# Performance work log

Measured on AMD Instinct MI355X. Metric: run time of the kernel, lower is better.

## Reference

```python
import jax, jax.numpy as jnp
import numpy as np

N_ATOMS = 100000
N_MOLS = 2500
MAX_NB = 10
HID = 256
ATOM_FDIM = 151
FEAT_DIM = 200
FFN_HID = 1024
N_TASKS = 12
LN_EPS = 1e-5


def setup_inputs() -> dict:
    key = jax.random.key(0)
    ks = jax.random.split(key, 12)
    atoms_per_mol = N_ATOMS // N_MOLS  # 40
    starts = jnp.arange(N_MOLS, dtype=jnp.int32) * atoms_per_mol
    sizes = jnp.full((N_MOLS,), atoms_per_mol, dtype=jnp.int32)
    a_scope = jnp.stack([starts, sizes], axis=1)  # [M, 2]
    d_in = HID + ATOM_FDIM  # 407
    d_ff = 4 * HID          # 1024
    d_mol_in = HID + FEAT_DIM  # 456
    def lin(k, fan_in, shape):
        return jax.random.uniform(k, shape, jnp.float32, -1.0, 1.0) / np.sqrt(fan_in)
    return {
        "atom_output": jax.random.normal(ks[0], (N_ATOMS, HID), jnp.float32),
        "original_f_atoms": jax.random.uniform(ks[1], (N_ATOMS, ATOM_FDIM), jnp.float32),
        "a2a": jax.random.randint(ks[2], (N_ATOMS, MAX_NB), 0, N_ATOMS, jnp.int32),
        "a_scope": a_scope,
        "features_batch": jax.random.normal(ks[3], (N_MOLS, FEAT_DIM), jnp.float32),
        "W1": lin(ks[4], d_in, (d_in, d_ff)), "b1": jnp.zeros((d_ff,), jnp.float32),
        "W2": lin(ks[5], d_ff, (d_ff, HID)), "b2": jnp.zeros((HID,), jnp.float32),
        "ln_g": jnp.ones((HID,), jnp.float32), "ln_b": jnp.zeros((HID,), jnp.float32),
        "Wm1": lin(ks[6], d_mol_in, (d_mol_in, FFN_HID)), "bm1": jnp.zeros((FFN_HID,), jnp.float32),
        "Wm2": lin(ks[7], FFN_HID, (FFN_HID, N_TASKS)), "bm2": jnp.zeros((N_TASKS,), jnp.float32),
    }


def reference(atom_output, original_f_atoms, a2a, a_scope, features_batch,
              W1, b1, W2, b2, ln_g, ln_b, Wm1, bm1, Wm2, bm2):
    # select_neighbor_and_aggregate: gather neighbor embeddings and sum
    aggr = atom_output[a2a].sum(axis=1)                      # [N, HID]
    x = jnp.concatenate([original_f_atoms, aggr], axis=1)    # [N, HID+ATOM_FDIM]
    # PositionwiseFeedForward (dropout = identity at eval)
    h = jax.nn.relu(x @ W1 + b1) @ W2 + b2                   # [N, HID]
    # SublayerConnection with x=None: LayerNorm (dropout identity)
    mu = h.mean(axis=-1, keepdims=True)
    var = ((h - mu) ** 2).mean(axis=-1, keepdims=True)
    h = (h - mu) * jax.lax.rsqrt(var + LN_EPS) * ln_g + ln_b
    # Readout: mean over variable-length a_scope ranges (segment mean)
    starts = a_scope[:, 0]
    sizes = a_scope[:, 1]
    n_mols = a_scope.shape[0]
    seg_ids = jnp.searchsorted(starts, jnp.arange(h.shape[0], dtype=starts.dtype), side="right") - 1
    sums = jax.ops.segment_sum(h, seg_ids, num_segments=n_mols)   # [M, HID]
    mol = sums / sizes[:, None].astype(h.dtype)
    # concat molecule-level features, then mol FFN (2 layers)
    mol = jnp.concatenate([mol, features_batch], axis=1)          # [M, HID+FEAT_DIM]
    out = jax.nn.relu(mol @ Wm1 + bm1) @ Wm2 + bm2                # [M, N_TASKS]
    return out
```

## Files before the change

kernel.cpp:

```cpp
#include <hip/hip_runtime.h>

typedef __attribute__((ext_vector_type(8))) short bfrag;
typedef __attribute__((ext_vector_type(4))) float f32x4;

__device__ __forceinline__ float bf2f(unsigned short u) {
    union { unsigned u32; float f; } cv; cv.u32 = ((unsigned)u) << 16; return cv.f;
}
__device__ __forceinline__ unsigned short f2bf(float f) {
    union { float f; unsigned u; } cv; cv.f = f;
    unsigned u = cv.u;
    unsigned r = (u + 0x7fffu + ((u >> 16) & 1u)) >> 16;
    return (unsigned short)r;
}
__device__ __forceinline__ void gll16(const void* g, void* l) {
    __builtin_amdgcn_global_load_lds(
        (const __attribute__((address_space(1))) unsigned int*)g,
        (__attribute__((address_space(3))) unsigned int*)l, 16, 0, 0);
}

__global__ void to_bf16(const float* __restrict__ src, unsigned short* __restrict__ dst, size_t n) {
    size_t i = ((size_t)blockIdx.x * 256 + threadIdx.x) * 8;
    if (i >= n) return;
    float4 a = *reinterpret_cast<const float4*>(src + i);
    float4 b = *reinterpret_cast<const float4*>(src + i + 4);
    ushort4 o0 = {f2bf(a.x), f2bf(a.y), f2bf(a.z), f2bf(a.w)};
    ushort4 o1 = {f2bf(b.x), f2bf(b.y), f2bf(b.z), f2bf(b.w)};
    *reinterpret_cast<ushort4*>(dst + i) = o0;
    *reinterpret_cast<ushort4*>(dst + i + 4) = o1;
}

__global__ void transpose_pad(const float* __restrict__ W, unsigned short* __restrict__ WT,
                              int R, int Cn, int Kp, int split, int shiftA, int split2, int shiftB) {
    __shared__ unsigned short tile[32][33];
    int r0 = blockIdx.x * 32, c0 = blockIdx.y * 32;
#pragma unroll
    for (int j = 0; j < 4; j++) {
        int r = r0 + threadIdx.y + j * 8;
        int c = c0 + threadIdx.x;
        float v = (r < R) ? W[(size_t)r * Cn + c] : 0.f;
        tile[threadIdx.y + j * 8][threadIdx.x] = f2bf(v);
    }
    __syncthreads();
#pragma unroll
    for (int j = 0; j < 4; j++) {
        int c = c0 + threadIdx.y + j * 8;
        int r = r0 + threadIdx.x;
        int kn = (r < split) ? r + shiftA : (r < split2 ? r + shiftB : r);
        WT[(size_t)c * Kp + kn] = tile[threadIdx.x][threadIdx.y + j * 8];
    }
}

__global__ __launch_bounds__(256) void gather2(const unsigned short* __restrict__ abf,
                                               const float* __restrict__ f_atoms,
                                               const int* __restrict__ a2a,
                                               unsigned short* __restrict__ xb, int n_real) {
    int r = blockIdx.x * 4 + (threadIdx.x >> 6);
    int lane = threadIdx.x & 63;
    unsigned short* xrow = xb + (size_t)r * 448;
    if (r >= n_real) {
        *reinterpret_cast<ushort4*>(xrow + lane * 4) = ushort4{0, 0, 0, 0};
        if (lane < 48) *reinterpret_cast<ushort4*>(xrow + 256 + lane * 4) = ushort4{0, 0, 0, 0};
        return;
    }
    int v = (lane < 10) ? a2a[(size_t)r * 10 + lane] : 0;
    ushort4 u[10];
#pragma unroll
    for (int j = 0; j < 10; j++) {
        int nbj = __shfl(v, j);
        u[j] = *reinterpret_cast<const ushort4*>(abf + (size_t)nbj * 256 + lane * 4);
    }
    float a0 = 0.f, a1 = 0.f, a2 = 0.f, a3 = 0.f;
#pragma unroll
    for (int j = 0; j < 10; j++) {
        a0 += bf2f(u[j].x);
        a1 += bf2f(u[j].y);
        a2 += bf2f(u[j].z);
        a3 += bf2f(u[j].w);
    }
    ushort4 o = {f2bf(a0), f2bf(a1), f2bf(a2), f2bf(a3)};
    *reinterpret_cast<ushort4*>(xrow + lane * 4) = o;
    const float* fr = f_atoms + (size_t)r * 151;
#pragma unroll
    for (int s = 0; s < 3; s++) {
        int c = lane + s * 64;
        if (c < 151) xrow[256 + c] = f2bf(fr[c]);
    }
    if (lane < 41) xrow[407 + lane] = 0;
}

template <int RELU>
__global__ __launch_bounds__(256) void gemm97(const unsigned short* __restrict__ A,
                                              const unsigned short* __restrict__ BT,
                                              const float* __restrict__ bias,
                                              unsigned short* __restrict__ C,
                                              int NB, int N, int K) {
    __shared__ __align__(16) unsigned short As[128 * 64];
    __shared__ __align__(16) unsigned short Bs[128 * 64];
    const int t = threadIdx.x;
    const int lane = t & 63, w = t >> 6;
    const int wr = w >> 1, wc = w & 1;
    const int la = lane & 15, hi = lane >> 4;

    const int nwg = gridDim.x, orig = blockIdx.x;
    const int q = nwg >> 3, r8 = nwg & 7;
    const int xcd = orig & 7, slot = orig >> 3;
    const int wgid = (xcd < r8 ? xcd * (q + 1) : r8 * (q + 1) + (xcd - r8) * q) + slot;
    const int bm = (wgid / NB) * 128, bn = (wgid % NB) * 128;

    f32x4 acc[4][4] = {};

    const int trow = t >> 3, tslot = t & 7;
    const unsigned short* Ag = A + (size_t)(bm + trow) * K + (tslot ^ (trow & 7)) * 8;
    const unsigned short* Bg = BT + (size_t)(bn + trow) * K + (tslot ^ (trow & 7)) * 8;
    const int ldst = trow * 64 + tslot * 8;

    for (int kt = 0; kt < K; kt += 64) {
        __builtin_amdgcn_s_barrier();
#pragma unroll
        for (int p = 0; p < 4; p++) gll16(Ag + (size_t)(p * 32) * K + kt, &As[p * 2048 + ldst]);
#pragma unroll
        for (int p = 0; p < 4; p++) gll16(Bg + (size_t)(p * 32) * K + kt, &Bs[p * 2048 + ldst]);
        asm volatile("s_waitcnt vmcnt(0)" ::: "memory");
        __builtin_amdgcn_s_barrier();
#pragma unroll
        for (int kk = 0; kk < 2; kk++) {
            bfrag a[4], b[4];
#pragma unroll
            for (int i = 0; i < 4; i++) {
                int row = wr * 64 + i * 16 + la;
                a[i] = *reinterpret_cast<const bfrag*>(&As[row * 64 + (((kk * 4 + hi) ^ (la & 7)) * 8)]);
            }
#pragma unroll
            for (int j = 0; j < 4; j++) {
                int row = wc * 64 + j * 16 + la;
                b[j] = *reinterpret_cast<const bfrag*>(&Bs[row * 64 + (((kk * 4 + hi) ^ (la & 7)) * 8)]);
            }
#pragma unroll
            for (int i = 0; i < 4; i++)
#pragma unroll
                for (int j = 0; j < 4; j++)
                    acc[i][j] = __builtin_amdgcn_mfma_f32_16x16x32_bf16(a[i], b[j], acc[i][j], 0, 0, 0);
        }
    }

#pragma unroll
    for (int j = 0; j < 4; j++) {
        int col = bn + wc * 64 + j * 16 + la;
        float bv = bias[col];
#pragma unroll
        for (int i = 0; i < 4; i++) {
            int rbase = bm + wr * 64 + i * 16 + hi * 4;
#pragma unroll
            for (int r = 0; r < 4; r++) {
                float v = acc[i][j][r] + bv;
                if (RELU) v = fmaxf(v, 0.f);
                C[(size_t)(rbase + r) * N + col] = f2bf(v);
            }
        }
    }
}

__global__ __launch_bounds__(512) void seg_ln_mean(const unsigned short* __restrict__ h,
                                                   const int* __restrict__ a_scope,
                                                   const float* __restrict__ g,
                                                   const float* __restrict__ b,
                                                   const float* __restrict__ feats,
                                                   unsigned short* __restrict__ mol, int n_mols) {
    __shared__ float part[8][256];
    int m = blockIdx.x, t = threadIdx.x;
    unsigned short* mrow = mol + (size_t)m * 512;
    if (m >= n_mols) {
        mrow[t] = 0;
        return;
    }
    int w = t >> 6, lane = t & 63;
    int start = a_scope[2 * m], size = a_scope[2 * m + 1];
    float4 gv = *reinterpret_cast<const float4*>(g + lane * 4);
    float4 bv = *reinterpret_cast<const float4*>(b + lane * 4);
    float a0 = 0.f, a1 = 0.f, a2 = 0.f, a3 = 0.f;
    for (int r = w; r < size; r += 8) {
        const unsigned short* hp = h + (size_t)(start + r) * 256 + lane * 4;
        ushort4 u = *reinterpret_cast<const ushort4*>(hp);
        float v0 = bf2f(u.x), v1 = bf2f(u.y), v2 = bf2f(u.z), v3 = bf2f(u.w);
        float s = v0 + v1 + v2 + v3;
        float q2 = v0 * v0 + v1 * v1 + v2 * v2 + v3 * v3;
#pragma unroll
        for (int off = 32; off; off >>= 1) {
            s += __shfl_xor(s, off);
            q2 += __shfl_xor(q2, off);
        }
        float mean = s * (1.f / 256.f);
        float var = q2 * (1.f / 256.f) - mean * mean;
        float rs = rsqrtf(var + 1e-5f);
        a0 += (v0 - mean) * rs * gv.x + bv.x;
        a1 += (v1 - mean) * rs * gv.y + bv.y;
        a2 += (v2 - mean) * rs * gv.z + bv.z;
        a3 += (v3 - mean) * rs * gv.w + bv.w;
    }
    part[w][lane * 4 + 0] = a0;
    part[w][lane * 4 + 1] = a1;
    part[w][lane * 4 + 2] = a2;
    part[w][lane * 4 + 3] = a3;
    __syncthreads();
    if (t < 256) {
        float sum = 0.f;
#pragma unroll
        for (int i = 0; i < 8; i++) sum += part[i][t];
        mrow[t] = f2bf(sum / (float)size);
    } else {
        int c = t - 256;
        float fv = (c < 200) ? feats[(size_t)m * 200 + c] : 0.f;
        mrow[256 + c] = f2bf(fv);
    }
}

__global__ void ffn2(const unsigned short* __restrict__ m1, const float* __restrict__ Wm2,
                     const float* __restrict__ bm2, float* __restrict__ out, int n_mols) {
    int wid = blockIdx.x * 4 + (threadIdx.x >> 6);
    if (wid >= n_mols) return;
    int lane = threadIdx.x & 63;
    float acc[12] = {};
    const unsigned short* row = m1 + (size_t)wid * 1024;
#pragma unroll 4
    for (int i = 0; i < 16; i++) {
        int k = i * 64 + lane;
        float v = bf2f(row[k]);
        const float* wr_ = Wm2 + (size_t)k * 12;
#pragma unroll
        for (int tsk = 0; tsk < 12; tsk++) acc[tsk] += v * wr_[tsk];
    }
#pragma unroll
    for (int tsk = 0; tsk < 12; tsk++) {
        float sv = acc[tsk];
#pragma unroll
        for (int off = 32; off; off >>= 1) sv += __shfl_xor(sv, off);
        if (lane == 0) out[(size_t)wid * 12 + tsk] = sv + bm2[tsk];
    }
}

extern "C" void kernel_launch(void* const* d_in, const int* in_sizes, int n_in,
                              void* d_out, int out_size, void* d_ws, size_t ws_size,
                              hipStream_t stream) {
    const float* atom_output = (const float*)d_in[0];
    const float* f_atoms     = (const float*)d_in[1];
    const int*   a2a         = (const int*)d_in[2];
    const int*   a_scope     = (const int*)d_in[3];
    const float* feats       = (const float*)d_in[4];
    const float* W1  = (const float*)d_in[5];
    const float* b1  = (const float*)d_in[6];
    const float* W2  = (const float*)d_in[7];
    const float* b2  = (const float*)d_in[8];
    const float* ln_g = (const float*)d_in[9];
    const float* ln_b = (const float*)d_in[10];
    const float* Wm1 = (const float*)d_in[11];
    const float* bm1 = (const float*)d_in[12];
    const float* Wm2 = (const float*)d_in[13];
    const float* bm2 = (const float*)d_in[14];
    float* out = (float*)d_out;

    char* ws = (char*)d_ws;
    size_t off = 0;
    auto alloc = [&](size_t bytes) {
        void* p = ws + off;
        off += (bytes + 255) & ~(size_t)255;
        return p;
    };
    unsigned short* h     = (unsigned short*)alloc((size_t)100096 * 256 * 2);
    unsigned short* h1    = (unsigned short*)alloc((size_t)100096 * 1024 * 2);
    unsigned short* xf    = (unsigned short*)alloc((size_t)100096 * 448 * 2);
    unsigned short* mol   = (unsigned short*)alloc((size_t)2560 * 512 * 2);
    unsigned short* m1b   = (unsigned short*)alloc((size_t)2560 * 1024 * 2);
    unsigned short* W1bT  = (unsigned short*)alloc((size_t)1024 * 448 * 2);
    unsigned short* W2bT  = (unsigned short*)alloc((size_t)256 * 1024 * 2);
    unsigned short* Wm1bT = (unsigned short*)alloc((size_t)1024 * 512 * 2);
    unsigned short* abf   = h1;

    transpose_pad<<<dim3(14, 32), dim3(32, 8), 0, stream>>>(W1, W1bT, 407, 1024, 448, 151, 256, 407, -151);
    transpose_pad<<<dim3(32, 8),  dim3(32, 8), 0, stream>>>(W2, W2bT, 1024, 256, 1024, 0, 0, 0, 0);
    transpose_pad<<<dim3(16, 32), dim3(32, 8), 0, stream>>>(Wm1, Wm1bT, 456, 1024, 512, 0, 0, 0, 0);

    to_bf16<<<12500, 256, 0, stream>>>(atom_output, abf, (size_t)100000 * 256);
    gather2<<<25024, 256, 0, stream>>>(abf, f_atoms, a2a, xf, 100000);

    gemm97<1><<<782 * 8, 256, 0, stream>>>(xf, W1bT, b1, h1, 8, 1024, 448);
    gemm97<0><<<782 * 2, 256, 0, stream>>>(h1, W2bT, b2, h, 2, 256, 1024);

    seg_ln_mean<<<2560, 512, 0, stream>>>(h, a_scope, ln_g, ln_b, feats, mol, 2500);
    gemm97<1><<<20 * 8, 256, 0, stream>>>(mol, Wm1bT, bm1, m1b, 8, 1024, 512);
    ffn2<<<625, 256, 0, stream>>>(m1b, Wm2, bm2, out, 2500);
}
```

Baseline: 434.1 us.

## Enlarge GEMM tile to 256x128 with 8 waves and widen neighbor gather loads

The GEMM kernel moves from 128x128 tiles with 4 waves to 256x128 tiles with 8 waves per 512-thread block, so each B tile loaded into LDS feeds twice as many rows. This cuts B-operand global traffic and the number of workgroups. The neighbor gather now uses 16-byte loads, with each half-wavefront summing five neighbors and then combining the halves through a cross-lane shuffle. The trade-offs are more LDS per block, which may limit occupancy, and padding concerns for the small mol GEMM (2560 rows, 10 row tiles of 256).

```diff
diff --git a/kernel.cpp b/kernel.cpp
--- a/kernel.cpp
+++ b/kernel.cpp
@@ -62,23 +62,24 @@
         if (lane < 48) *reinterpret_cast<ushort4*>(xrow + 256 + lane * 4) = ushort4{0, 0, 0, 0};
         return;
     }
+    const int half = lane >> 5, lq = lane & 31;
     int v = (lane < 10) ? a2a[(size_t)r * 10 + lane] : 0;
-    ushort4 u[10];
-#pragma unroll
-    for (int j = 0; j < 10; j++) {
-        int nbj = __shfl(v, j);
-        u[j] = *reinterpret_cast<const ushort4*>(abf + (size_t)nbj * 256 + lane * 4);
-    }
-    float a0 = 0.f, a1 = 0.f, a2 = 0.f, a3 = 0.f;
-#pragma unroll
-    for (int j = 0; j < 10; j++) {
-        a0 += bf2f(u[j].x);
-        a1 += bf2f(u[j].y);
-        a2 += bf2f(u[j].z);
-        a3 += bf2f(u[j].w);
-    }
-    ushort4 o = {f2bf(a0), f2bf(a1), f2bf(a2), f2bf(a3)};
-    *reinterpret_cast<ushort4*>(xrow + lane * 4) = o;
+    float acc[8] = {};
+#pragma unroll
+    for (int jj = 0; jj < 5; jj++) {
+        int nbj = __shfl(v, jj * 2 + half);
+        bfrag u = *reinterpret_cast<const bfrag*>(abf + (size_t)nbj * 256 + lq * 8);
+#pragma unroll
+        for (int k = 0; k < 8; k++) acc[k] += bf2f((unsigned short)u[k]);
+    }
+#pragma unroll
+    for (int k = 0; k < 8; k++) acc[k] += __shfl_xor(acc[k], 32);
+    if (half == 0) {
+        bfrag o;
+#pragma unroll
+        for (int k = 0; k < 8; k++) o[k] = (short)f2bf(acc[k]);
+        *reinterpret_cast<bfrag*>(xrow + lq * 8) = o;
+    }
     const float* fr = f_atoms + (size_t)r * 151;
 #pragma unroll
     for (int s = 0; s < 3; s++) {
@@ -89,37 +90,37 @@
 }
 
 template <int RELU>
-__global__ __launch_bounds__(256) void gemm97(const unsigned short* __restrict__ A,
-                                              const unsigned short* __restrict__ BT,
-                                              const float* __restrict__ bias,
-                                              unsigned short* __restrict__ C,
-                                              int NB, int N, int K) {
-    __shared__ __align__(16) unsigned short As[128 * 64];
+__global__ __launch_bounds__(512, 2) void gemm256(const unsigned short* __restrict__ A,
+                                                  const unsigned short* __restrict__ BT,
+                                                  const float* __restrict__ bias,
+                                                  unsigned short* __restrict__ C,
+                                                  int NB, int N, int K) {
+    __shared__ __align__(16) unsigned short As[256 * 64];
     __shared__ __align__(16) unsigned short Bs[128 * 64];
     const int t = threadIdx.x;
-    const int lane = t & 63, w = t >> 6;
-    const int wr = w >> 1, wc = w & 1;
+    const int lane = t & 63, wid = t >> 6;
+    const int wm = wid >> 1, wn = wid & 1;
     const int la = lane & 15, hi = lane >> 4;
 
     const int nwg = gridDim.x, orig = blockIdx.x;
     const int q = nwg >> 3, r8 = nwg & 7;
     const int xcd = orig & 7, slot = orig >> 3;
     const int wgid = (xcd < r8 ? xcd * (q + 1) : r8 * (q + 1) + (xcd - r8) * q) + slot;
-    const int bm = (wgid / NB) * 128, bn = (wgid % NB) * 128;
+    const int bm = (wgid / NB) * 256, bn = (wgid % NB) * 128;
 
     f32x4 acc[4][4] = {};
 
-    const int trow = t >> 3, tslot = t & 7;
-    const unsigned short* Ag = A + (size_t)(bm + trow) * K + (tslot ^ (trow & 7)) * 8;
-    const unsigned short* Bg = BT + (size_t)(bn + trow) * K + (tslot ^ (trow & 7)) * 8;
-    const int ldst = trow * 64 + tslot * 8;
+    const int tr = t >> 3, ts = t & 7;
+    const unsigned short* Ag = A + (size_t)(bm + tr) * K + (ts ^ (tr & 7)) * 8;
+    const unsigned short* Bg = BT + (size_t)(bn + tr) * K + (ts ^ (tr & 7)) * 8;
+    const int ldst = tr * 64 + ts * 8;
 
     for (int kt = 0; kt < K; kt += 64) {
         __builtin_amdgcn_s_barrier();
 #pragma unroll
-        for (int p = 0; p < 4; p++) gll16(Ag + (size_t)(p * 32) * K + kt, &As[p * 2048 + ldst]);
-#pragma unroll
-        for (int p = 0; p < 4; p++) gll16(Bg + (size_t)(p * 32) * K + kt, &Bs[p * 2048 + ldst]);
+        for (int p = 0; p < 4; p++) gll16(Ag + (size_t)(p * 64) * K + kt, &As[p * 4096 + ldst]);
+#pragma unroll
+        for (int p = 0; p < 2; p++) gll16(Bg + (size_t)(p * 64) * K + kt, &Bs[p * 4096 + ldst]);
         asm volatile("s_waitcnt vmcnt(0)" ::: "memory");
         __builtin_amdgcn_s_barrier();
 #pragma unroll
@@ -127,12 +128,12 @@
             bfrag a[4], b[4];
 #pragma unroll
             for (int i = 0; i < 4; i++) {
-                int row = wr * 64 + i * 16 + la;
+                int row = wm * 64 + i * 16 + la;
                 a[i] = *reinterpret_cast<const bfrag*>(&As[row * 64 + (((kk * 4 + hi) ^ (la & 7)) * 8)]);
             }
 #pragma unroll
             for (int j = 0; j < 4; j++) {
-                int row = wc * 64 + j * 16 + la;
+                int row = wn * 64 + j * 16 + la;
                 b[j] = *reinterpret_cast<const bfrag*>(&Bs[row * 64 + (((kk * 4 + hi) ^ (la & 7)) * 8)]);
             }
 #pragma unroll
@@ -145,11 +146,11 @@
 
 #pragma unroll
     for (int j = 0; j < 4; j++) {
-        int col = bn + wc * 64 + j * 16 + la;
+        int col = bn + wn * 64 + j * 16 + la;
         float bv = bias[col];
 #pragma unroll
         for (int i = 0; i < 4; i++) {
-            int rbase = bm + wr * 64 + i * 16 + hi * 4;
+            int rbase = bm + wm * 64 + i * 16 + hi * 4;
 #pragma unroll
             for (int r = 0; r < 4; r++) {
                 float v = acc[i][j][r] + bv;
@@ -282,10 +283,10 @@
     to_bf16<<<12500, 256, 0, stream>>>(atom_output, abf, (size_t)100000 * 256);
     gather2<<<25024, 256, 0, stream>>>(abf, f_atoms, a2a, xf, 100000);
 
-    gemm97<1><<<782 * 8, 256, 0, stream>>>(xf, W1bT, b1, h1, 8, 1024, 448);
-    gemm97<0><<<782 * 2, 256, 0, stream>>>(h1, W2bT, b2, h, 2, 256, 1024);
+    gemm256<1><<<391 * 8, 512, 0, stream>>>(xf, W1bT, b1, h1, 8, 1024, 448);
+    gemm256<0><<<391 * 2, 512, 0, stream>>>(h1, W2bT, b2, h, 2, 256, 1024);
 
     seg_ln_mean<<<2560, 512, 0, stream>>>(h, a_scope, ln_g, ln_b, feats, mol, 2500);
-    gemm97<1><<<20 * 8, 256, 0, stream>>>(mol, Wm1bT, bm1, m1b, 8, 1024, 512);
+    gemm256<1><<<10 * 8, 512, 0, stream>>>(mol, Wm1bT, bm1, m1b, 8, 1024, 512);
     ffn2<<<625, 256, 0, stream>>>(m1b, Wm2, bm2, out, 2500);
 }
```

Result: faster. 392.3 us, median of 4 (-9.6%).
